# Optimization experiments

Measured on AMD Instinct MI355X. Metric: run time of the kernel, lower is better.

Reference implementation:

```python
import jax, jax.numpy as jnp
import numpy as np

HEAD_DIM = 64
SCALE = 1.0 / np.sqrt(HEAD_DIM).astype(np.float32)


def setup_inputs() -> dict:
    key = jax.random.key(0)
    k1, k2 = jax.random.split(key)
    B, S, D = 4, 4096, 1024
    x = jax.random.normal(k1, (B, S, D), dtype=jnp.float32)
    wq = jax.random.normal(k2, (HEAD_DIM, D), dtype=jnp.float32) * (1.0 / np.sqrt(D))
    return {"x": x, "wq": wq}


def reference(x, wq):
    # Faithful to the original forward: wq is (buggily) used for q, k AND v.
    q = jnp.einsum('bsd,hd->bsh', x, wq)   # [B, S, 64]
    k = q
    v = q
    scores = jnp.einsum('bqh,bkh->bqk', q, k) * SCALE  # [B, S, S]
    attn = jax.nn.softmax(scores, axis=-1)
    out = jnp.einsum('bqk,bkh->bqh', attn, v)          # [B, S, 64]
    return out
```

## Files before the change

### kernel.cpp

```cpp
#include <hip/hip_runtime.h>
#include <hip/hip_bf16.h>

#define B_ 4
#define S_ 4096
#define D_ 1024
#define H_ 64
#define SCALE_ 0.125f
#define CFAC_ 0.180336884f
#define WP_ 1056
#define SP_ 4224
#define NSPLIT 8

typedef __attribute__((ext_vector_type(8))) short bf16x8;
typedef __attribute__((ext_vector_type(4))) float f32x4;

static __device__ __forceinline__ short f2bf(float f) {
    unsigned u = __builtin_bit_cast(unsigned, f);
    u += 0x7fffu + ((u >> 16) & 1u);
    return (short)(u >> 16);
}

static __device__ __forceinline__ unsigned pk_trunc(float f0, float f1) {
    return (__builtin_bit_cast(unsigned, f1) & 0xffff0000u)
         | (__builtin_bit_cast(unsigned, f0) >> 16);
}

__global__ __launch_bounds__(256) void winit_kernel(
    const float* __restrict__ wq, short* __restrict__ wqb)
{
    const int i   = blockIdx.x * 256 + threadIdx.x;
    const int row = i >> 7;
    const int col = (i & 127) * 8;
    const float* s = wq + (size_t)row * D_ + col;
    bf16x8 v;
#pragma unroll
    for (int e = 0; e < 8; ++e) v[e] = f2bf(s[e]);
    *(bf16x8*)(wqb + (size_t)row * WP_ + col) = v;
}

__global__ __launch_bounds__(256) void qproj_mfma(
    const float* __restrict__ x, const short* __restrict__ wqb,
    short* __restrict__ q, short* __restrict__ qT, short* __restrict__ qsb)
{
    __shared__ short xs[4][16][264];
    __shared__ float cs[4][16][68];
    __shared__ short qs[16][68];

    const int tid  = threadIdx.x;
    const int wave = tid >> 6;
    const int lane = tid & 63;
    const int quad = lane >> 4;
    const int lr   = lane & 15;
    const int row0 = blockIdx.x * 16;

    {
        const float* xp = x + (size_t)row0 * D_ + wave * 256 + lane * 4;
#pragma unroll
        for (int s = 0; s < 16; ++s) {
            const f32x4 v = *(const f32x4*)(xp + (size_t)s * D_);
            unsigned long long pk = 0;
#pragma unroll
            for (int e = 0; e < 4; ++e)
                pk |= (unsigned long long)(unsigned short)f2bf(v[e]) << (16 * e);
            *(unsigned long long*)&xs[wave][s][lane * 4] = pk;
        }
    }
    __syncthreads();

    f32x4 acc[4];
#pragma unroll
    for (int nb = 0; nb < 4; ++nb) acc[nb] = (f32x4){0.f, 0.f, 0.f, 0.f};

    const short* wp = wqb + (size_t)lr * WP_ + wave * 256 + quad * 8;
#pragma unroll
    for (int t = 0; t < 8; ++t) {
        const bf16x8 a = *(const bf16x8*)&xs[wave][lr][t * 32 + quad * 8];
#pragma unroll
        for (int nb = 0; nb < 4; ++nb) {
            const bf16x8 bb = *(const bf16x8*)(wp + (size_t)(nb * 16) * WP_ + t * 32);
            acc[nb] = __builtin_amdgcn_mfma_f32_16x16x32_bf16(a, bb, acc[nb], 0, 0, 0);
        }
    }

#pragma unroll
    for (int nb = 0; nb < 4; ++nb)
#pragma unroll
        for (int i = 0; i < 4; ++i)
            cs[wave][quad * 4 + i][nb * 16 + lr] = acc[nb][i];
    __syncthreads();

    const int r  = tid >> 4;
    const int c4 = (tid & 15) * 4;
    unsigned long long pv = 0, pw = 0;
#pragma unroll
    for (int j = 0; j < 4; ++j) {
        const float s = cs[0][r][c4 + j] + cs[1][r][c4 + j]
                      + cs[2][r][c4 + j] + cs[3][r][c4 + j];
        pv |= (unsigned long long)(unsigned short)f2bf(s) << (16 * j);
        pw |= (unsigned long long)(unsigned short)f2bf(s * CFAC_) << (16 * j);
    }
    *(unsigned long long*)(q   + (size_t)(row0 + r) * H_ + c4) = pv;
    *(unsigned long long*)(qsb + (size_t)(row0 + r) * H_ + c4) = pw;
    *(unsigned long long*)&qs[r][c4] = pv;
    __syncthreads();

    const int hh = tid >> 2;
    const int sj = (tid & 3) * 4;
    const int b  = row0 >> 12;
    const int sl = row0 & (S_ - 1);
    unsigned long long w = 0;
#pragma unroll
    for (int e = 0; e < 4; ++e)
        w |= (unsigned long long)(unsigned short)qs[sj + e][hh] << (16 * e);
    *(unsigned long long*)(qT + ((size_t)b * H_ + hh) * SP_ + sl + sj) = w;
}

__global__ __launch_bounds__(256, 4) void flash_mfma(
    const short* __restrict__ q, const short* __restrict__ qT,
    const short* __restrict__ qsb,
    float* __restrict__ opart, float* __restrict__ lbuf)
{
    __shared__ short kt[64 * 64];
    __shared__ short vt[64 * 64];
    __shared__ short plT[4][2][16][72];

    const int tid  = threadIdx.x;
    const int w    = tid >> 6;
    const int lane = tid & 63;
    const int quad = lane >> 4;
    const int lr   = lane & 15;
    const int b    = blockIdx.y;
    const int q0   = blockIdx.x * 128;
    const int z    = blockIdx.z;
    const int slice = S_ / gridDim.z;
    const int kbase = z * slice;
    const short* qb  = q  + (size_t)b * S_ * H_;
    const short* qTb = qT + (size_t)b * H_ * SP_;

    bf16x8 qB[2][2];
#pragma unroll
    for (int qs = 0; qs < 2; ++qs) {
        const short* qr = qsb + (size_t)(b * S_ + q0 + w * 32 + qs * 16 + lr) * H_;
        qB[qs][0] = *(const bf16x8*)(qr + quad * 8);
        qB[qs][1] = *(const bf16x8*)(qr + 32 + quad * 8);
    }

    bf16x8 ones;
#pragma unroll
    for (int e = 0; e < 8; ++e) ones[e] = (short)0x3f80;

    f32x4 o[2][4];
#pragma unroll
    for (int qs = 0; qs < 2; ++qs)
#pragma unroll
        for (int mt = 0; mt < 4; ++mt) o[qs][mt] = (f32x4){0.f, 0.f, 0.f, 0.f};
    f32x4 lsum[2];
    lsum[0] = (f32x4){0.f, 0.f, 0.f, 0.f};
    lsum[1] = (f32x4){0.f, 0.f, 0.f, 0.f};

    const int srow = tid >> 2;
    const int g0   = (tid & 3) * 2;
    const int sw0  = (g0 ^ (srow & 7)) * 8;
    const int sw1  = ((g0 + 1) ^ (srow & 7)) * 8;
    const short* gk = qb  + (size_t)(kbase + srow) * H_ + g0 * 8;
    const short* gv = qTb + (size_t)srow * SP_ + kbase + g0 * 8;

    uint4 pk0 = *(const uint4*)gk, pk1 = *(const uint4*)(gk + 8);
    uint4 pv0 = *(const uint4*)gv, pv1 = *(const uint4*)(gv + 8);

    const int iters = slice >> 6;
    for (int it = 0; it < iters; ++it) {
        __syncthreads();
        *(uint4*)&kt[srow * 64 + sw0] = pk0;
        *(uint4*)&kt[srow * 64 + sw1] = pk1;
        *(uint4*)&vt[srow * 64 + sw0] = pv0;
        *(uint4*)&vt[srow * 64 + sw1] = pv1;
        __syncthreads();
        if (it + 1 < iters) {
            gk += (size_t)64 * H_;
            gv += 64;
            pk0 = *(const uint4*)gk; pk1 = *(const uint4*)(gk + 8);
            pv0 = *(const uint4*)gv; pv1 = *(const uint4*)(gv + 8);
        }

#pragma unroll
        for (int mp = 0; mp < 2; ++mp) {
            f32x4 s[2][2];
            s[0][0] = (f32x4){0.f, 0.f, 0.f, 0.f};
            s[0][1] = (f32x4){0.f, 0.f, 0.f, 0.f};
            s[1][0] = (f32x4){0.f, 0.f, 0.f, 0.f};
            s[1][1] = (f32x4){0.f, 0.f, 0.f, 0.f};
#pragma unroll
            for (int c = 0; c < 2; ++c)
#pragma unroll
                for (int m2 = 0; m2 < 2; ++m2) {
                    const int row = (mp * 2 + m2) * 16 + lr;
                    const bf16x8 a = *(const bf16x8*)&kt[row * 64 + (((c * 4 + quad) ^ (row & 7)) * 8)];
                    s[0][m2] = __builtin_amdgcn_mfma_f32_16x16x32_bf16(a, qB[0][c], s[0][m2], 0, 0, 0);
                    s[1][m2] = __builtin_amdgcn_mfma_f32_16x16x32_bf16(a, qB[1][c], s[1][m2], 0, 0, 0);
                }
#pragma unroll
            for (int qs = 0; qs < 2; ++qs)
#pragma unroll
                for (int m2 = 0; m2 < 2; ++m2) {
                    const int mt = mp * 2 + m2;
                    const float p0 = __builtin_amdgcn_exp2f(s[qs][m2][0]);
                    const float p1 = __builtin_amdgcn_exp2f(s[qs][m2][1]);
                    const float p2 = __builtin_amdgcn_exp2f(s[qs][m2][2]);
                    const float p3 = __builtin_amdgcn_exp2f(s[qs][m2][3]);
                    unsigned lohi[2];
                    lohi[0] = pk_trunc(p0, p1);
                    lohi[1] = pk_trunc(p2, p3);
                    *(unsigned long long*)&plT[w][qs][lr][mt * 16 + quad * 4] =
                        *(unsigned long long*)lohi;
                }
        }

#pragma unroll
        for (int c = 0; c < 2; ++c) {
            const bf16x8 pB0 = *(const bf16x8*)&plT[w][0][lr][c * 32 + quad * 8];
            const bf16x8 pB1 = *(const bf16x8*)&plT[w][1][lr][c * 32 + quad * 8];
            lsum[0] = __builtin_amdgcn_mfma_f32_16x16x32_bf16(ones, pB0, lsum[0], 0, 0, 0);
            lsum[1] = __builtin_amdgcn_mfma_f32_16x16x32_bf16(ones, pB1, lsum[1], 0, 0, 0);
#pragma unroll
            for (int mt = 0; mt < 4; ++mt) {
                const int row = mt * 16 + lr;
                const bf16x8 a = *(const bf16x8*)&vt[row * 64 + (((c * 4 + quad) ^ (row & 7)) * 8)];
                o[0][mt] = __builtin_amdgcn_mfma_f32_16x16x32_bf16(a, pB0, o[0][mt], 0, 0, 0);
                o[1][mt] = __builtin_amdgcn_mfma_f32_16x16x32_bf16(a, pB1, o[1][mt], 0, 0, 0);
            }
        }
    }

#pragma unroll
    for (int qs = 0; qs < 2; ++qs) {
        float* ob = opart + (((size_t)z * B_ + b) * S_ + q0 + w * 32 + qs * 16 + lr) * H_;
#pragma unroll
        for (int mt = 0; mt < 4; ++mt)
            *(f32x4*)(ob + mt * 16 + quad * 4) = o[qs][mt];
        if (quad == 0)
            lbuf[((size_t)z * B_ + b) * S_ + q0 + w * 32 + qs * 16 + lr] = lsum[qs][0];
    }
}

__global__ __launch_bounds__(256) void combine_kernel(
    const float* __restrict__ opart, const float* __restrict__ lbuf,
    float* __restrict__ out, int nsplit)
{
    const int t   = blockIdx.x * 256 + threadIdx.x;
    const int row = t >> 4;
    const int c4  = (t & 15) * 4;
    f32x4 acc = (f32x4){0.f, 0.f, 0.f, 0.f};
    float l = 0.0f;
    for (int z = 0; z < nsplit; ++z) {
        const f32x4 v = *(const f32x4*)(opart + ((size_t)z * (B_ * S_) + row) * H_ + c4);
        acc[0] += v[0]; acc[1] += v[1]; acc[2] += v[2]; acc[3] += v[3];
        l += lbuf[(size_t)z * (B_ * S_) + row];
    }
    const float r = 1.0f / l;
    acc[0] *= r; acc[1] *= r; acc[2] *= r; acc[3] *= r;
    *(f32x4*)(out + (size_t)row * H_ + c4) = acc;
}

extern "C" void kernel_launch(void* const* d_in, const int* in_sizes, int n_in,
                              void* d_out, int out_size, void* d_ws, size_t ws_size,
                              hipStream_t stream) {
    const float* x  = (const float*)d_in[0];
    const float* wq = (const float*)d_in[1];
    float* out = (float*)d_out;

    const size_t off_qT  = 2097152;
    const size_t off_wqb = off_qT + (size_t)B_ * H_ * SP_ * 2;
    const size_t off_qsb = off_wqb + (size_t)H_ * WP_ * 2;
    const size_t off_op  = off_qsb + 2097152;
    short* qbuf = (short*)d_ws;
    short* qT   = (short*)((char*)d_ws + off_qT);
    short* wqb  = (short*)((char*)d_ws + off_wqb);
    short* qsb  = (short*)((char*)d_ws + off_qsb);

    const size_t per_split = (size_t)B_ * S_ * H_ * 4 + (size_t)B_ * S_ * 4;
    int nsplit = NSPLIT;
    while (nsplit > 1 && ws_size < off_op + (size_t)nsplit * per_split) nsplit >>= 1;
    float* opart = (float*)((char*)d_ws + off_op);
    float* lbuf  = (float*)((char*)d_ws + off_op + (size_t)nsplit * B_ * S_ * H_ * 4);

    winit_kernel<<<dim3(32), dim3(256), 0, stream>>>(wq, wqb);
    qproj_mfma<<<dim3((B_ * S_) / 16), dim3(256), 0, stream>>>(x, wqb, qbuf, qT, qsb);
    flash_mfma<<<dim3(S_ / 128, B_, nsplit), dim3(256), 0, stream>>>(qbuf, qT, qsb, opart, lbuf);
    combine_kernel<<<dim3(1024), dim3(256), 0, stream>>>(opart, lbuf, out, nsplit);
}
```

Before: 134.6 us.

## Double-buffer K/V LDS tiles and halve the key-split count

K and V tiles in shared memory become double-buffered, so the next tile is written into the alternate buffer after compute and the loop needs one barrier per iteration instead of two. NSPLIT is also cut from 8 to 4, so there are fewer, longer blocks along the key axis and less partial output for the combine step to write and read. The cost is double the LDS for K/V, which may lower occupancy, and fewer blocks in flight to fill the GPU.

```diff
diff --git a/kernel.cpp b/kernel.cpp
--- a/kernel.cpp
+++ b/kernel.cpp
@@ -9,7 +9,7 @@
 #define CFAC_ 0.180336884f
 #define WP_ 1056
 #define SP_ 4224
-#define NSPLIT 8
+#define NSPLIT 4
 
 typedef __attribute__((ext_vector_type(8))) short bf16x8;
 typedef __attribute__((ext_vector_type(4))) float f32x4;
@@ -120,8 +120,8 @@
     const short* __restrict__ qsb,
     float* __restrict__ opart, float* __restrict__ lbuf)
 {
-    __shared__ short kt[64 * 64];
-    __shared__ short vt[64 * 64];
+    __shared__ short kt[2][64 * 64];
+    __shared__ short vt[2][64 * 64];
     __shared__ short plT[4][2][16][72];
 
     const int tid  = threadIdx.x;
@@ -165,23 +165,26 @@
     const short* gk = qb  + (size_t)(kbase + srow) * H_ + g0 * 8;
     const short* gv = qTb + (size_t)srow * SP_ + kbase + g0 * 8;
 
+    const int iters = slice >> 6;
+
     uint4 pk0 = *(const uint4*)gk, pk1 = *(const uint4*)(gk + 8);
     uint4 pv0 = *(const uint4*)gv, pv1 = *(const uint4*)(gv + 8);
-
-    const int iters = slice >> 6;
+    *(uint4*)&kt[0][srow * 64 + sw0] = pk0;
+    *(uint4*)&kt[0][srow * 64 + sw1] = pk1;
+    *(uint4*)&vt[0][srow * 64 + sw0] = pv0;
+    *(uint4*)&vt[0][srow * 64 + sw1] = pv1;
+    if (iters > 1) {
+        gk += (size_t)64 * H_;
+        gv += 64;
+        pk0 = *(const uint4*)gk; pk1 = *(const uint4*)(gk + 8);
+        pv0 = *(const uint4*)gv; pv1 = *(const uint4*)(gv + 8);
+    }
+    __syncthreads();
+
     for (int it = 0; it < iters; ++it) {
-        __syncthreads();
-        *(uint4*)&kt[srow * 64 + sw0] = pk0;
-        *(uint4*)&kt[srow * 64 + sw1] = pk1;
-        *(uint4*)&vt[srow * 64 + sw0] = pv0;
-        *(uint4*)&vt[srow * 64 + sw1] = pv1;
-        __syncthreads();
-        if (it + 1 < iters) {
-            gk += (size_t)64 * H_;
-            gv += 64;
-            pk0 = *(const uint4*)gk; pk1 = *(const uint4*)(gk + 8);
-            pv0 = *(const uint4*)gv; pv1 = *(const uint4*)(gv + 8);
-        }
+        const int cur = it & 1;
+        const short* ktc = kt[cur];
+        const short* vtc = vt[cur];
 
 #pragma unroll
         for (int mp = 0; mp < 2; ++mp) {
@@ -195,7 +198,7 @@
 #pragma unroll
                 for (int m2 = 0; m2 < 2; ++m2) {
                     const int row = (mp * 2 + m2) * 16 + lr;
-                    const bf16x8 a = *(const bf16x8*)&kt[row * 64 + (((c * 4 + quad) ^ (row & 7)) * 8)];
+                    const bf16x8 a = *(const bf16x8*)&ktc[row * 64 + (((c * 4 + quad) ^ (row & 7)) * 8)];
                     s[0][m2] = __builtin_amdgcn_mfma_f32_16x16x32_bf16(a, qB[0][c], s[0][m2], 0, 0, 0);
                     s[1][m2] = __builtin_amdgcn_mfma_f32_16x16x32_bf16(a, qB[1][c], s[1][m2], 0, 0, 0);
                 }
@@ -225,11 +228,26 @@
 #pragma unroll
             for (int mt = 0; mt < 4; ++mt) {
                 const int row = mt * 16 + lr;
-                const bf16x8 a = *(const bf16x8*)&vt[row * 64 + (((c * 4 + quad) ^ (row & 7)) * 8)];
+                const bf16x8 a = *(const bf16x8*)&vtc[row * 64 + (((c * 4 + quad) ^ (row & 7)) * 8)];
                 o[0][mt] = __builtin_amdgcn_mfma_f32_16x16x32_bf16(a, pB0, o[0][mt], 0, 0, 0);
                 o[1][mt] = __builtin_amdgcn_mfma_f32_16x16x32_bf16(a, pB1, o[1][mt], 0, 0, 0);
             }
         }
+
+        if (it + 1 < iters) {
+            const int nxt = cur ^ 1;
+            *(uint4*)&kt[nxt][srow * 64 + sw0] = pk0;
+            *(uint4*)&kt[nxt][srow * 64 + sw1] = pk1;
+            *(uint4*)&vt[nxt][srow * 64 + sw0] = pv0;
+            *(uint4*)&vt[nxt][srow * 64 + sw1] = pv1;
+            if (it + 2 < iters) {
+                gk += (size_t)64 * H_;
+                gv += 64;
+                pk0 = *(const uint4*)gk; pk1 = *(const uint4*)(gk + 8);
+                pv0 = *(const uint4*)gv; pv1 = *(const uint4*)(gv + 8);
+            }
+        }
+        __syncthreads();
     }
 
 #pragma unroll
```

New measurement: 134.3 us. Within noise of the previous version (-0.2%).
